# Optimization experiments

Hardware: AMD Instinct MI355X
Metric: run time of the kernel (lower is better)

The kernel has to match this reference:

```python
import jax, jax.numpy as jnp
import numpy as np

D_MODEL = 512
NUM_HEADS = 8
HEAD_DIM = D_MODEL // NUM_HEADS


def setup_inputs() -> dict:
    key = jax.random.key(0)
    ks = jax.random.split(key, 11)
    N, S, D = 2, 4096, D_MODEL
    s = 1.0 / np.sqrt(D)
    return {
        "query": jax.random.normal(ks[0], (N, S, D), jnp.float32),
        "key": jax.random.normal(ks[1], (N, S, D), jnp.float32),
        "value": jax.random.normal(ks[2], (N, S, D), jnp.float32),
        "Wq": jax.random.normal(ks[3], (D, D), jnp.float32) * s,
        "bq": jnp.zeros((D,), jnp.float32),
        "Wk": jax.random.normal(ks[4], (D, D), jnp.float32) * s,
        "bk": jnp.zeros((D,), jnp.float32),
        "Wv": jax.random.normal(ks[5], (D, D), jnp.float32) * s,
        "bv": jnp.zeros((D,), jnp.float32),
        "Wo": jax.random.normal(ks[6], (D, D), jnp.float32) * s,
        "bo": jnp.zeros((D,), jnp.float32),
    }


def reference(query, key, value, Wq, bq, Wk, bk, Wv, bv, Wo, bo):
    N, S, D = query.shape
    H, Hd = NUM_HEADS, HEAD_DIM
    # Linear projections (torch Linear: x @ W.T + b), split heads -> [N,H,S,Hd]
    Q = (query @ Wq.T + bq).reshape(N, S, H, Hd).transpose(0, 2, 1, 3)
    K = (key @ Wk.T + bk).reshape(N, S, H, Hd).transpose(0, 2, 1, 3)
    V = (value @ Wv.T + bv).reshape(N, S, H, Hd).transpose(0, 2, 1, 3)
    scale = 1.0 / np.sqrt(Hd)
    energy = jnp.einsum("nhqd,nhkd->nhqk", Q, K) * scale  # [N,H,S,S]
    attention = jax.nn.softmax(energy, axis=-1)
    out = jnp.einsum("nhqk,nhkd->nhqd", attention, V)
    out = out.transpose(0, 2, 1, 3).reshape(N, S, D)
    return out @ Wo.T + bo
```

## Files before the change

### kernel.cpp

```cpp
#include <hip/hip_runtime.h>


#define SEQ 4096
#define PERHEAD 262144
#define CEXPF 0.18033688011112042f

typedef short bf16x8 __attribute__((ext_vector_type(8)));
typedef short bf16x4 __attribute__((ext_vector_type(4)));
typedef float f32x4 __attribute__((ext_vector_type(4)));
typedef unsigned short u16;
typedef unsigned int u32;

__device__ inline float bf2f(u16 h) {
    return __uint_as_float(((u32)h) << 16);
}
__device__ inline u16 f2bf(float f) {
    u32 u = __float_as_uint(f);
    u = (u + 0x7fffu + ((u >> 16) & 1u)) >> 16;
    return (u16)u;
}
__device__ inline u32 packtrunc(float lo, float hi) {
    return __builtin_amdgcn_perm(__float_as_uint(hi), __float_as_uint(lo),
                                 0x07060302u);
}
__device__ inline uint4 pack8(float4 a, float4 b) {
    uint4 r;
    r.x = (u32)f2bf(a.x) | ((u32)f2bf(a.y) << 16);
    r.y = (u32)f2bf(a.z) | ((u32)f2bf(a.w) << 16);
    r.z = (u32)f2bf(b.x) | ((u32)f2bf(b.y) << 16);
    r.w = (u32)f2bf(b.z) | ((u32)f2bf(b.w) << 16);
    return r;
}

__device__ inline int detect_f32(const void* W) {
    const int lane = threadIdx.x & 63;
    u16 uu = ((const u16*)W)[2 * lane];
    int e = (uu >> 7) & 0xFF;
    int plaus = (uu == 0) || (e >= 100 && e <= 132);
    unsigned long long m = __ballot(plaus);
    return (__popcll(m) >= 48) ? 0 : 1;
}

template <int A_BF16, int BM, int BN>
__device__ inline void gemm_body(
    const void* __restrict__ Av, const void* __restrict__ Bv,
    const void* __restrict__ biasv, void* __restrict__ outv,
    int isf32, int mode, float scale, int m0, int n0,
    u16* As, u16* Bs)
{
    constexpr int MI = BM / 32;
    constexpr int NI = BN / 32;
    constexpr int TPRA = 256 / BM;
    constexpr int TA = 64 / TPRA;
    constexpr int TPRB = 256 / BN;
    constexpr int TB = 64 / TPRB;
    const int tid = threadIdx.x;
    const int wave = tid >> 6, lane = tid & 63, quad = lane >> 4, ln = lane & 15;
    const int qr = wave >> 1, qc = wave & 1;

    f32x4 acc[MI][NI];
#pragma unroll
    for (int i = 0; i < MI; i++)
#pragma unroll
        for (int j = 0; j < NI; j++) acc[i][j] = (f32x4){0.f, 0.f, 0.f, 0.f};

    const int arow = tid / TPRA;
    const int acol = (tid % TPRA) * TA;
    const int brow = tid / TPRB;
    const int bcol = (tid % TPRB) * TB;
    const uint4*  Ag16 = (const uint4*) ((const u16*)Av + (size_t)(m0 + arow) * 512 + acol);
    const float4* Ag32 = (const float4*)((const float*)Av + (size_t)(m0 + arow) * 512 + acol);
    const uint4*  Bg16 = (const uint4*) ((const u16*)Bv + (size_t)(n0 + brow) * 512 + bcol);
    const float4* Bg32 = (const float4*)((const float*)Bv + (size_t)(n0 + brow) * 512 + bcol);
    uint4* Al = (uint4*)(As + arow * 72 + acol);
    uint4* Bl = (uint4*)(Bs + brow * 72 + bcol);

    for (int kk = 0; kk < 512; kk += 64) {
        __syncthreads();
        uint4 aw[TA / 8], bw[TB / 8];
        if (A_BF16 || !isf32) {
#pragma unroll
            for (int j = 0; j < TA / 8; j++) aw[j] = Ag16[j];
        } else {
            float4 fv[TA / 4];
#pragma unroll
            for (int j = 0; j < TA / 4; j++) fv[j] = Ag32[j];
#pragma unroll
            for (int j = 0; j < TA / 8; j++) aw[j] = pack8(fv[2 * j], fv[2 * j + 1]);
        }
        Ag16 += 8; Ag32 += 16;
        if (!isf32) {
#pragma unroll
            for (int j = 0; j < TB / 8; j++) bw[j] = Bg16[j];
        } else {
            float4 fv[TB / 4];
#pragma unroll
            for (int j = 0; j < TB / 4; j++) fv[j] = Bg32[j];
#pragma unroll
            for (int j = 0; j < TB / 8; j++) bw[j] = pack8(fv[2 * j], fv[2 * j + 1]);
        }
        Bg16 += 8; Bg32 += 16;
#pragma unroll
        for (int j = 0; j < TA / 8; j++) Al[j] = aw[j];
#pragma unroll
        for (int j = 0; j < TB / 8; j++) Bl[j] = bw[j];
        __syncthreads();
#pragma unroll
        for (int ks = 0; ks < 2; ks++) {
            bf16x8 af[MI], bfr[NI];
#pragma unroll
            for (int mi = 0; mi < MI; mi++)
                af[mi] = *(const bf16x8*)(As + (qr * (BM / 2) + mi * 16 + ln) * 72 +
                                          ks * 32 + quad * 8);
#pragma unroll
            for (int ni = 0; ni < NI; ni++)
                bfr[ni] = *(const bf16x8*)(Bs + (qc * (BN / 2) + ni * 16 + ln) * 72 +
                                           ks * 32 + quad * 8);
#pragma unroll
            for (int mi = 0; mi < MI; mi++)
#pragma unroll
                for (int ni = 0; ni < NI; ni++)
                    acc[mi][ni] = __builtin_amdgcn_mfma_f32_16x16x32_bf16(
                        af[mi], bfr[ni], acc[mi][ni], 0, 0, 0);
        }
    }

#pragma unroll
    for (int ni = 0; ni < NI; ni++) {
        const int col = n0 + qc * (BN / 2) + ni * 16 + ln;
        const float bvv = isf32 ? ((const float*)biasv)[col]
                                : bf2f(((const u16*)biasv)[col]);
#pragma unroll
        for (int mi = 0; mi < MI; mi++) {
#pragma unroll
            for (int r = 0; r < 4; r++) {
                const int row = m0 + qr * (BM / 2) + mi * 16 + quad * 4 + r;
                const float v = (acc[mi][ni][r] + bvv) * scale;
                if (mode == 0) {
                    const size_t idx = (size_t)row * 512 + col;
                    if (isf32) ((float*)outv)[idx] = v;
                    else       ((u16*)outv)[idx] = f2bf(v);
                } else {
                    const int b = row >> 12, s = row & 4095;
                    const int h = col >> 6, hd = col & 63;
                    size_t idx;
                    if (mode == 1) {
                        idx = (size_t)(b * 8 + h) * PERHEAD + (size_t)s * 64 + hd;
                    } else {
                        const int s6 = s & 63;
                        const int p = (s6 & 32) | ((s6 & 12) << 1) |
                                      ((s6 & 16) >> 2) | (s6 & 3);
                        idx = (size_t)(b * 8 + h) * PERHEAD + (size_t)hd * 4096 +
                              (size_t)((s & ~63) + p);
                    }
                    ((u16*)outv)[idx] = f2bf(v);
                }
            }
        }
    }
}

__global__ __launch_bounds__(256, 3) void qkv_proj(
    const void* __restrict__ q, const void* __restrict__ k, const void* __restrict__ v,
    const void* __restrict__ Wq, const void* __restrict__ Wk, const void* __restrict__ Wv,
    const void* __restrict__ bq, const void* __restrict__ bk, const void* __restrict__ bv,
    u16* __restrict__ Qh, u16* __restrict__ Kh, u16* __restrict__ Vt)
{
    __shared__ __align__(16) u16 As[128 * 72];
    __shared__ __align__(16) u16 Bs[128 * 72];
    const int g = blockIdx.x + 4 * (blockIdx.y + 64 * blockIdx.z);
    const int l = (g & 7) * 96 + (g >> 3);
    const int bx = l & 3;
    const int by = (l >> 2) & 63;
    const int z = l >> 8;
    const void* Av = (z == 0) ? q : (z == 1) ? k : v;
    const void* Wz = (z == 0) ? Wq : (z == 1) ? Wk : Wv;
    const void* bz = (z == 0) ? bq : (z == 1) ? bk : bv;
    void* outv = (z == 0) ? (void*)Qh : (z == 1) ? (void*)Kh : (void*)Vt;
    const int mode = (z == 2) ? 2 : 1;
    const float scale = (z == 0) ? CEXPF : 1.0f;
    const int isf32 = detect_f32(Wz);
    gemm_body<0, 128, 128>(Av, Wz, bz, outv, isf32, mode, scale,
                           by * 128, bx * 128, As, Bs);
}

__global__ __launch_bounds__(256, 4) void out_proj(
    const void* __restrict__ Av, const void* __restrict__ Wo,
    const void* __restrict__ bo, void* __restrict__ outv)
{
    __shared__ __align__(16) u16 As[64 * 72];
    __shared__ __align__(16) u16 Bs[64 * 72];
    const int g = blockIdx.x + 8 * blockIdx.y;
    const int l = (g & 7) * 128 + (g >> 3);
    const int bx = l & 7;
    const int by = l >> 3;
    const int isf32 = detect_f32(Wo);
    gemm_body<1, 64, 64>(Av, Wo, bo, outv, isf32, 0, 1.0f,
                         by * 64, bx * 64, As, Bs);
}

__global__ __launch_bounds__(512) void attn_kernel(
    const u16* __restrict__ Q, const u16* __restrict__ K,
    const u16* __restrict__ Vt, u16* __restrict__ AO)
{
    __shared__ __align__(16) u16 SM[19456];

    const int tid = threadIdx.x;
    const int gw = tid >> 8;
    const int wq = (tid >> 6) & 3;
    const int lane = tid & 63, quad = lane >> 4, ln = lane & 15;
    const int gblk = blockIdx.x + 32 * blockIdx.y;
    const int lblk = (gblk & 7) * 64 + (gblk >> 3);
    const int bh = lblk >> 5;
    const int q0 = (lblk & 31) * 128;
    const size_t base = (size_t)bh * PERHEAD;

    bf16x8 qf[2][2];
#pragma unroll
    for (int qt = 0; qt < 2; qt++) {
        const uint4* qp = (const uint4*)(Q + base + (size_t)(q0 + wq * 32 + qt * 16 + ln) * 64);
        uint4 v0 = qp[quad], v1 = qp[4 + quad];
        qf[qt][0] = *(bf16x8*)&v0;
        qf[qt][1] = *(bf16x8*)&v1;
    }

    bf16x8 ones;
#pragma unroll
    for (int j = 0; j < 8; j++) ones[j] = (short)0x3F80;

    f32x4 oT[2][4];
    f32x4 lacc[2];
#pragma unroll
    for (int qt = 0; qt < 2; qt++) {
        lacc[qt] = (f32x4){0.f, 0.f, 0.f, 0.f};
#pragma unroll
        for (int mt = 0; mt < 4; mt++) oT[qt][mt] = (f32x4){0.f, 0.f, 0.f, 0.f};
    }

    const int tid2 = tid & 255;
    const int srowK = tid2 >> 3, scK = (tid2 & 7) * 8;
    const int srowV = tid2 >> 2, scV = (tid2 & 3) * 8;
    const uint4* Kg = (const uint4*)(K + base + (size_t)(gw * 2048 + srowK) * 64 + scK);
    const uint4* Vg = (const uint4*)(Vt + base + (size_t)srowV * 4096 + gw * 2048 + scV);
    const int kloff = srowK * 72 + scK;
    const int vloff = srowV * 40 + scV;

    {
        uint4 a = Kg[0], c = Vg[0];
        Kg += 256; Vg += 4;
        *(uint4*)(SM + (gw * 2 + 0) * 2304 + kloff) = a;
        *(uint4*)(SM + 9216 + (gw * 2 + 0) * 2560 + vloff) = c;
    }
    __syncthreads();

    for (int it = 0; it < 64; ++it) {
        const u16* Kc = SM + (gw * 2 + (it & 1)) * 2304;
        const u16* Vc = SM + 9216 + (gw * 2 + (it & 1)) * 2560;

        uint4 pa = Kg[0], pc = Vg[0];
        Kg += 256; Vg += 4;

        f32x4 s[2][2];
        __builtin_amdgcn_s_setprio(1);
#pragma unroll
        for (int t = 0; t < 2; t++)
#pragma unroll
            for (int kt = 0; kt < 2; kt++) {
                bf16x8 kf = *(const bf16x8*)(Kc + (kt * 16 + ln) * 72 + t * 32 + quad * 8);
#pragma unroll
                for (int qt = 0; qt < 2; qt++) {
                    if (t == 0)
                        s[qt][kt] = __builtin_amdgcn_mfma_f32_16x16x32_bf16(
                            kf, qf[qt][0], (f32x4){0.f, 0.f, 0.f, 0.f}, 0, 0, 0);
                    else
                        s[qt][kt] = __builtin_amdgcn_mfma_f32_16x16x32_bf16(
                            kf, qf[qt][1], s[qt][kt], 0, 0, 0);
                }
            }
        __builtin_amdgcn_s_setprio(0);

        bf16x8 pf[2];
#pragma unroll
        for (int qt = 0; qt < 2; qt++) {
            float e0 = __builtin_amdgcn_exp2f(s[qt][0][0]);
            float e1 = __builtin_amdgcn_exp2f(s[qt][0][1]);
            float e2 = __builtin_amdgcn_exp2f(s[qt][0][2]);
            float e3 = __builtin_amdgcn_exp2f(s[qt][0][3]);
            float f0 = __builtin_amdgcn_exp2f(s[qt][1][0]);
            float f1 = __builtin_amdgcn_exp2f(s[qt][1][1]);
            float f2 = __builtin_amdgcn_exp2f(s[qt][1][2]);
            float f3 = __builtin_amdgcn_exp2f(s[qt][1][3]);
            u32 w0 = packtrunc(e0, e1), w1 = packtrunc(e2, e3);
            u32 w2 = packtrunc(f0, f1), w3 = packtrunc(f2, f3);
            uint4 pk = {w0, w1, w2, w3};
            pf[qt] = *(bf16x8*)&pk;
        }

        __builtin_amdgcn_s_setprio(1);
#pragma unroll
        for (int qt = 0; qt < 2; qt++)
            lacc[qt] = __builtin_amdgcn_mfma_f32_16x16x32_bf16(
                ones, pf[qt], lacc[qt], 0, 0, 0);

#pragma unroll
        for (int mt = 0; mt < 4; mt++) {
            bf16x8 vf = *(const bf16x8*)(Vc + (mt * 16 + ln) * 40 + quad * 8);
#pragma unroll
            for (int qt = 0; qt < 2; qt++)
                oT[qt][mt] = __builtin_amdgcn_mfma_f32_16x16x32_bf16(
                    vf, pf[qt], oT[qt][mt], 0, 0, 0);
        }
        __builtin_amdgcn_s_setprio(0);

        *(uint4*)(SM + (gw * 2 + ((it + 1) & 1)) * 2304 + kloff) = pa;
        *(uint4*)(SM + 9216 + (gw * 2 + ((it + 1) & 1)) * 2560 + vloff) = pc;
        __syncthreads();
    }

    float* Xch = (float*)SM;
    if (gw == 1) {
#pragma unroll
        for (int qt = 0; qt < 2; qt++) {
#pragma unroll
            for (int mt = 0; mt < 4; mt++)
#pragma unroll
                for (int r = 0; r < 4; r++)
                    Xch[(((wq * 2 + qt) * 4 + mt) * 16 + quad * 4 + r) * 17 + ln] =
                        oT[qt][mt][r];
            if (quad == 0)
                Xch[8704 + (wq * 2 + qt) * 16 + ln] = lacc[qt][0];
        }
    }
    __syncthreads();
    if (gw == 0) {
        const int b = bh >> 3, h = bh & 7;
#pragma unroll
        for (int qt = 0; qt < 2; qt++) {
            const float l2 = Xch[8704 + (wq * 2 + qt) * 16 + ln];
            const float inv = 1.0f / (lacc[qt][0] + l2);
            const int qrow = q0 + wq * 32 + qt * 16 + ln;
            u16* op = AO + (size_t)(b * 4096 + qrow) * 512 + h * 64 + quad * 4;
#pragma unroll
            for (int mt = 0; mt < 4; mt++) {
                float o0 = oT[qt][mt][0] +
                    Xch[(((wq * 2 + qt) * 4 + mt) * 16 + quad * 4 + 0) * 17 + ln];
                float o1 = oT[qt][mt][1] +
                    Xch[(((wq * 2 + qt) * 4 + mt) * 16 + quad * 4 + 1) * 17 + ln];
                float o2 = oT[qt][mt][2] +
                    Xch[(((wq * 2 + qt) * 4 + mt) * 16 + quad * 4 + 2) * 17 + ln];
                float o3 = oT[qt][mt][3] +
                    Xch[(((wq * 2 + qt) * 4 + mt) * 16 + quad * 4 + 3) * 17 + ln];
                uint2 pk;
                pk.x = (u32)f2bf(o0 * inv) | ((u32)f2bf(o1 * inv) << 16);
                pk.y = (u32)f2bf(o2 * inv) | ((u32)f2bf(o3 * inv) << 16);
                *(uint2*)(op + mt * 16) = pk;
            }
        }
    }
}

extern "C" void kernel_launch(void* const* d_in, const int* in_sizes, int n_in,
                              void* d_out, int out_size, void* d_ws, size_t ws_size,
                              hipStream_t stream)
{
    (void)in_sizes; (void)n_in; (void)out_size; (void)ws_size;
    const void* q  = d_in[0];
    const void* k  = d_in[1];
    const void* v  = d_in[2];
    const void* Wq = d_in[3];
    const void* bq = d_in[4];
    const void* Wk = d_in[5];
    const void* bk = d_in[6];
    const void* Wv = d_in[7];
    const void* bv = d_in[8];
    const void* Wo = d_in[9];
    const void* bo = d_in[10];

    u16* ws = (u16*)d_ws;
    u16* Kh = ws;
    u16* Vt = ws + 4194304;
    u16* AO = ws + 8388608;
    u16* Qh = (u16*)d_out;

    qkv_proj<<<dim3(4, 64, 3), 256, 0, stream>>>(q, k, v, Wq, Wk, Wv,
                                                 bq, bk, bv, Qh, Kh, Vt);
    attn_kernel<<<dim3(32, 16), 512, 0, stream>>>(Qh, Kh, Vt, AO);
    out_proj<<<dim3(8, 128), 256, 0, stream>>>(AO, Wo, bo, d_out);
}
```

Measured before the change: 245.7 us.

## Double-buffer projection GEMM LDS tiles and retile QKV projection to 128x64

```diff
diff --git a/kernel.cpp b/kernel.cpp
--- a/kernel.cpp
+++ b/kernel.cpp
@@ -42,7 +42,7 @@
 }
 
 template <int A_BF16, int BM, int BN>
-__device__ inline void gemm_body(
+__device__ inline void gemm_dbuf(
     const void* __restrict__ Av, const void* __restrict__ Bv,
     const void* __restrict__ biasv, void* __restrict__ outv,
     int isf32, int mode, float scale, int m0, int n0,
@@ -50,10 +50,12 @@
 {
     constexpr int MI = BM / 32;
     constexpr int NI = BN / 32;
-    constexpr int TPRA = 256 / BM;
-    constexpr int TA = 64 / TPRA;
-    constexpr int TPRB = 256 / BN;
-    constexpr int TB = 64 / TPRB;
+    constexpr int TRA = 256 / BM;
+    constexpr int CA = 32 / TRA;
+    constexpr int NA = CA / 8;
+    constexpr int TRB = 256 / BN;
+    constexpr int CB = 32 / TRB;
+    constexpr int NB = CB / 8;
     const int tid = threadIdx.x;
     const int wave = tid >> 6, lane = tid & 63, quad = lane >> 4, ln = lane & 15;
     const int qr = wave >> 1, qc = wave & 1;
@@ -64,65 +66,85 @@
 #pragma unroll
         for (int j = 0; j < NI; j++) acc[i][j] = (f32x4){0.f, 0.f, 0.f, 0.f};
 
-    const int arow = tid / TPRA;
-    const int acol = (tid % TPRA) * TA;
-    const int brow = tid / TPRB;
-    const int bcol = (tid % TPRB) * TB;
-    const uint4*  Ag16 = (const uint4*) ((const u16*)Av + (size_t)(m0 + arow) * 512 + acol);
-    const float4* Ag32 = (const float4*)((const float*)Av + (size_t)(m0 + arow) * 512 + acol);
-    const uint4*  Bg16 = (const uint4*) ((const u16*)Bv + (size_t)(n0 + brow) * 512 + bcol);
-    const float4* Bg32 = (const float4*)((const float*)Bv + (size_t)(n0 + brow) * 512 + bcol);
-    uint4* Al = (uint4*)(As + arow * 72 + acol);
-    uint4* Bl = (uint4*)(Bs + brow * 72 + bcol);
-
-    for (int kk = 0; kk < 512; kk += 64) {
+    const int arow = tid / TRA;
+    const int acol = (tid % TRA) * CA;
+    const int brow = tid / TRB;
+    const int bcol = (tid % TRB) * CB;
+    const u16*   A16 = (const u16*)Av;
+    const float* A32 = (const float*)Av;
+    const u16*   B16 = (const u16*)Bv;
+    const float* B32 = (const float*)Bv;
+    const size_t abase = (size_t)(m0 + arow) * 512 + acol;
+    const size_t bbase = (size_t)(n0 + brow) * 512 + bcol;
+    const int aoff = arow * 40 + acol;
+    const int boff = brow * 40 + bcol;
+
+    auto load_tiles = [&](int ka, uint4* aw, uint4* bw) {
+        if (A_BF16 || !isf32) {
+#pragma unroll
+            for (int j = 0; j < NA; j++)
+                aw[j] = *(const uint4*)(A16 + abase + ka + j * 8);
+        } else {
+            float4 fv[2 * NA];
+#pragma unroll
+            for (int j = 0; j < 2 * NA; j++)
+                fv[j] = *(const float4*)(A32 + abase + ka + j * 4);
+#pragma unroll
+            for (int j = 0; j < NA; j++) aw[j] = pack8(fv[2 * j], fv[2 * j + 1]);
+        }
+        if (!isf32) {
+#pragma unroll
+            for (int j = 0; j < NB; j++)
+                bw[j] = *(const uint4*)(B16 + bbase + ka + j * 8);
+        } else {
+            float4 fv[2 * NB];
+#pragma unroll
+            for (int j = 0; j < 2 * NB; j++)
+                fv[j] = *(const float4*)(B32 + bbase + ka + j * 4);
+#pragma unroll
+            for (int j = 0; j < NB; j++) bw[j] = pack8(fv[2 * j], fv[2 * j + 1]);
+        }
+    };
+
+    {
+        uint4 aw[NA], bw[NB];
+        load_tiles(0, aw, bw);
+#pragma unroll
+        for (int j = 0; j < NA; j++) *(uint4*)(As + aoff + j * 8) = aw[j];
+#pragma unroll
+        for (int j = 0; j < NB; j++) *(uint4*)(Bs + boff + j * 8) = bw[j];
+    }
+    __syncthreads();
+
+    int ka = 32;
+    for (int it = 0; it < 16; ++it) {
+        uint4 aw[NA], bw[NB];
+        load_tiles(ka, aw, bw);
+        if (ka < 480) ka += 32;
+
+        const u16* Ac = As + (it & 1) * (BM * 40);
+        const u16* Bc = Bs + (it & 1) * (BN * 40);
+        bf16x8 af[MI], bfr[NI];
+#pragma unroll
+        for (int mi = 0; mi < MI; mi++)
+            af[mi] = *(const bf16x8*)(Ac + (qr * (BM / 2) + mi * 16 + ln) * 40 + quad * 8);
+#pragma unroll
+        for (int ni = 0; ni < NI; ni++)
+            bfr[ni] = *(const bf16x8*)(Bc + (qc * (BN / 2) + ni * 16 + ln) * 40 + quad * 8);
+#pragma unroll
+        for (int mi = 0; mi < MI; mi++)
+#pragma unroll
+            for (int ni = 0; ni < NI; ni++)
+                acc[mi][ni] = __builtin_amdgcn_mfma_f32_16x16x32_bf16(
+                    af[mi], bfr[ni], acc[mi][ni], 0, 0, 0);
+
+        u16* Aw = As + ((it + 1) & 1) * (BM * 40);
+        u16* Bw = Bs + ((it + 1) & 1) * (BN * 40);
+#pragma unroll
+        for (int j = 0; j < NA; j++) *(uint4*)(Aw + aoff + j * 8) = aw[j];
+#pragma unroll
+        for (int j = 0; j < NB; j++) *(uint4*)(Bw + boff + j * 8) = bw[j];
         __syncthreads();
-        uint4 aw[TA / 8], bw[TB / 8];
-        if (A_BF16 || !isf32) {
-#pragma unroll
-            for (int j = 0; j < TA / 8; j++) aw[j] = Ag16[j];
-        } else {
-            float4 fv[TA / 4];
-#pragma unroll
-            for (int j = 0; j < TA / 4; j++) fv[j] = Ag32[j];
-#pragma unroll
-            for (int j = 0; j < TA / 8; j++) aw[j] = pack8(fv[2 * j], fv[2 * j + 1]);
-        }
-        Ag16 += 8; Ag32 += 16;
-        if (!isf32) {
-#pragma unroll
-            for (int j = 0; j < TB / 8; j++) bw[j] = Bg16[j];
-        } else {
-            float4 fv[TB / 4];
-#pragma unroll
-            for (int j = 0; j < TB / 4; j++) fv[j] = Bg32[j];
-#pragma unroll
-            for (int j = 0; j < TB / 8; j++) bw[j] = pack8(fv[2 * j], fv[2 * j + 1]);
-        }
-        Bg16 += 8; Bg32 += 16;
-#pragma unroll
-        for (int j = 0; j < TA / 8; j++) Al[j] = aw[j];
-#pragma unroll
-        for (int j = 0; j < TB / 8; j++) Bl[j] = bw[j];
-        __syncthreads();
-#pragma unroll
-        for (int ks = 0; ks < 2; ks++) {
-            bf16x8 af[MI], bfr[NI];
-#pragma unroll
-            for (int mi = 0; mi < MI; mi++)
-                af[mi] = *(const bf16x8*)(As + (qr * (BM / 2) + mi * 16 + ln) * 72 +
-                                          ks * 32 + quad * 8);
-#pragma unroll
-            for (int ni = 0; ni < NI; ni++)
-                bfr[ni] = *(const bf16x8*)(Bs + (qc * (BN / 2) + ni * 16 + ln) * 72 +
-                                           ks * 32 + quad * 8);
-#pragma unroll
-            for (int mi = 0; mi < MI; mi++)
-#pragma unroll
-                for (int ni = 0; ni < NI; ni++)
-                    acc[mi][ni] = __builtin_amdgcn_mfma_f32_16x16x32_bf16(
-                        af[mi], bfr[ni], acc[mi][ni], 0, 0, 0);
-        }
     }
 
 #pragma unroll
@@ -132,47 +154,58 @@
                                 : bf2f(((const u16*)biasv)[col]);
 #pragma unroll
         for (int mi = 0; mi < MI; mi++) {
-#pragma unroll
-            for (int r = 0; r < 4; r++) {
-                const int row = m0 + qr * (BM / 2) + mi * 16 + quad * 4 + r;
-                const float v = (acc[mi][ni][r] + bvv) * scale;
-                if (mode == 0) {
-                    const size_t idx = (size_t)row * 512 + col;
-                    if (isf32) ((float*)outv)[idx] = v;
-                    else       ((u16*)outv)[idx] = f2bf(v);
+            const int row0 = m0 + qr * (BM / 2) + mi * 16 + quad * 4;
+            float v0 = (acc[mi][ni][0] + bvv) * scale;
+            float v1 = (acc[mi][ni][1] + bvv) * scale;
+            float v2 = (acc[mi][ni][2] + bvv) * scale;
+            float v3 = (acc[mi][ni][3] + bvv) * scale;
+            if (mode == 0) {
+                const size_t idx = (size_t)row0 * 512 + col;
+                if (isf32) {
+                    float* o = (float*)outv;
+                    o[idx] = v0; o[idx + 512] = v1;
+                    o[idx + 1024] = v2; o[idx + 1536] = v3;
                 } else {
-                    const int b = row >> 12, s = row & 4095;
-                    const int h = col >> 6, hd = col & 63;
-                    size_t idx;
-                    if (mode == 1) {
-                        idx = (size_t)(b * 8 + h) * PERHEAD + (size_t)s * 64 + hd;
-                    } else {
-                        const int s6 = s & 63;
-                        const int p = (s6 & 32) | ((s6 & 12) << 1) |
-                                      ((s6 & 16) >> 2) | (s6 & 3);
-                        idx = (size_t)(b * 8 + h) * PERHEAD + (size_t)hd * 4096 +
-                              (size_t)((s & ~63) + p);
-                    }
-                    ((u16*)outv)[idx] = f2bf(v);
+                    u16* o = (u16*)outv;
+                    o[idx] = f2bf(v0); o[idx + 512] = f2bf(v1);
+                    o[idx + 1024] = f2bf(v2); o[idx + 1536] = f2bf(v3);
+                }
+            } else {
+                const int b = row0 >> 12, s = row0 & 4095;
+                const int h = col >> 6, hd = col & 63;
+                if (mode == 1) {
+                    u16* o = (u16*)outv + (size_t)(b * 8 + h) * PERHEAD +
+                             (size_t)s * 64 + hd;
+                    o[0] = f2bf(v0); o[64] = f2bf(v1);
+                    o[128] = f2bf(v2); o[192] = f2bf(v3);
+                } else {
+                    const int s6 = s & 63;
+                    const int p = (s6 & 32) | ((s6 & 12) << 1) | ((s6 & 16) >> 2);
+                    u16* o = (u16*)outv + (size_t)(b * 8 + h) * PERHEAD +
+                             (size_t)hd * 4096 + (size_t)((s & ~63) + p);
+                    uint2 pk;
+                    pk.x = (u32)f2bf(v0) | ((u32)f2bf(v1) << 16);
+                    pk.y = (u32)f2bf(v2) | ((u32)f2bf(v3) << 16);
+                    *(uint2*)o = pk;
                 }
             }
         }
     }
 }
 
-__global__ __launch_bounds__(256, 3) void qkv_proj(
+__global__ __launch_bounds__(256, 5) void qkv_proj(
     const void* __restrict__ q, const void* __restrict__ k, const void* __restrict__ v,
     const void* __restrict__ Wq, const void* __restrict__ Wk, const void* __restrict__ Wv,
     const void* __restrict__ bq, const void* __restrict__ bk, const void* __restrict__ bv,
     u16* __restrict__ Qh, u16* __restrict__ Kh, u16* __restrict__ Vt)
 {
-    __shared__ __align__(16) u16 As[128 * 72];
-    __shared__ __align__(16) u16 Bs[128 * 72];
-    const int g = blockIdx.x + 4 * (blockIdx.y + 64 * blockIdx.z);
-    const int l = (g & 7) * 96 + (g >> 3);
-    const int bx = l & 3;
-    const int by = (l >> 2) & 63;
-    const int z = l >> 8;
+    __shared__ __align__(16) u16 As[2 * 128 * 40];
+    __shared__ __align__(16) u16 Bs[2 * 64 * 40];
+    const int gz = blockIdx.x + 8 * blockIdx.y;
+    const int l = (gz & 7) * 64 + (gz >> 3);
+    const int bx = l & 7;
+    const int by = l >> 3;
+    const int z = blockIdx.z;
     const void* Av = (z == 0) ? q : (z == 1) ? k : v;
     const void* Wz = (z == 0) ? Wq : (z == 1) ? Wk : Wv;
     const void* bz = (z == 0) ? bq : (z == 1) ? bk : bv;
@@ -180,22 +213,22 @@
     const int mode = (z == 2) ? 2 : 1;
     const float scale = (z == 0) ? CEXPF : 1.0f;
     const int isf32 = detect_f32(Wz);
-    gemm_body<0, 128, 128>(Av, Wz, bz, outv, isf32, mode, scale,
-                           by * 128, bx * 128, As, Bs);
+    gemm_dbuf<0, 128, 64>(Av, Wz, bz, outv, isf32, mode, scale,
+                          by * 128, bx * 64, As, Bs);
 }
 
 __global__ __launch_bounds__(256, 4) void out_proj(
     const void* __restrict__ Av, const void* __restrict__ Wo,
     const void* __restrict__ bo, void* __restrict__ outv)
 {
-    __shared__ __align__(16) u16 As[64 * 72];
-    __shared__ __align__(16) u16 Bs[64 * 72];
+    __shared__ __align__(16) u16 As[2 * 64 * 40];
+    __shared__ __align__(16) u16 Bs[2 * 64 * 40];
     const int g = blockIdx.x + 8 * blockIdx.y;
     const int l = (g & 7) * 128 + (g >> 3);
     const int bx = l & 7;
     const int by = l >> 3;
     const int isf32 = detect_f32(Wo);
-    gemm_body<1, 64, 64>(Av, Wo, bo, outv, isf32, 0, 1.0f,
+    gemm_dbuf<1, 64, 64>(Av, Wo, bo, outv, isf32, 0, 1.0f,
                          by * 64, bx * 64, As, Bs);
 }
 
@@ -382,7 +415,7 @@
     u16* AO = ws + 8388608;
     u16* Qh = (u16*)d_out;
 
-    qkv_proj<<<dim3(4, 64, 3), 256, 0, stream>>>(q, k, v, Wq, Wk, Wv,
+    qkv_proj<<<dim3(8, 64, 3), 256, 0, stream>>>(q, k, v, Wq, Wk, Wv,
                                                  bq, bk, bv, Qh, Kh, Vt);
     attn_kernel<<<dim3(32, 16), 512, 0, stream>>>(Qh, Kh, Vt, AO);
     out_proj<<<dim3(8, 128), 256, 0, stream>>>(AO, Wo, bo, d_out);
```

After: 241.6 us. About the same (-1.7%).
